# Kernel tuning notes

Measured on AMD Instinct MI355X. Metric: run time of the kernel, lower is better.

## Reference

```python
import jax, jax.numpy as jnp
import numpy as np

# PyTorch LSTM cell with zero initial (h, c): W_hh @ h0 == 0, and c = sigmoid(i)*tanh(g)
# since the forget-gate term f*c0 vanishes. Gate order in torch: i, f, g, o.
# b here is the combined b_ih + b_hh (identical math).

def lstm_step0(x, Wih, b):
    pre = x @ Wih.T + b                      # (N, 4H)
    i, f, g, o = jnp.split(pre, 4, axis=-1)
    c = jax.nn.sigmoid(i) * jnp.tanh(g)
    return jax.nn.sigmoid(o) * jnp.tanh(c)   # (N, H)


def setup_inputs() -> dict:
    key = jax.random.key(0)
    ks = jax.random.split(key, 13)
    num_ts, num_periods, F = 128, 256, 128
    GH, NH, NF = 512, 256, 10
    s = lambda k, shape, fan: (jax.random.normal(k, shape, jnp.float32) / np.sqrt(fan))
    return {
        "X": jax.random.normal(ks[0], (num_ts, num_periods, F), jnp.float32),
        "g_Wih0": s(ks[1], (4 * GH, F), F),
        "g_b0": s(ks[2], (4 * GH,), GH),
        "g_Wih1": s(ks[3], (4 * GH, GH), GH),
        "g_b1": s(ks[4], (4 * GH,), GH),
        "aff_W": s(ks[5], (NF, GH), GH),
        "aff_b": s(ks[6], (NF,), GH),
        "n_Wih0": s(ks[7], (4 * NH, F), F),
        "n_b0": s(ks[8], (4 * NH,), NH),
        "n_Wih1": s(ks[9], (4 * NH, NH), NH),
        "n_b1": s(ks[10], (4 * NH,), NH),
        "noise_W": s(ks[11], (1, NH), NH),
        "noise_b": s(ks[12], (1,), NH),
    }


def reference(X, g_Wih0, g_b0, g_Wih1, g_b1, aff_W, aff_b,
              n_Wih0, n_b0, n_Wih1, n_b1, noise_W, noise_b):
    num_ts, num_periods, num_feats = X.shape
    x = X.reshape(-1, num_feats)             # (num_ts*num_periods, F)

    # Global factor branch: 2-layer LSTM single step from zero state
    hg = lstm_step0(lstm_step0(x, g_Wih0, g_b0), g_Wih1, g_b1)
    hg = jax.nn.relu(hg)
    mus = (hg @ aff_W.T + aff_b).sum(axis=-1).reshape(num_ts, num_periods)

    # Noise branch: 2-layer LSTM single step from zero state
    hn = lstm_step0(lstm_step0(x, n_Wih0, n_b0), n_Wih1, n_b1)
    hn = jax.nn.relu(hn)
    sigmas = jax.nn.softplus(hn @ noise_W.T + noise_b)  # log(1+exp(.)), stable
    sigmas = sigmas.reshape(num_ts, num_periods) + 1e-6
    return mus, sigmas
```

## Files before the change

### kernel.cpp

```cpp
#include <hip/hip_runtime.h>
#include <hip/hip_bf16.h>
#include <hip/hip_fp16.h>

typedef _Float16 h8_t __attribute__((ext_vector_type(8)));
typedef _Float16 h4_t __attribute__((ext_vector_type(4)));
typedef float f4_t __attribute__((ext_vector_type(4)));

#define M_ROWS 32768

__device__ __forceinline__ void gload_lds16(const void* g, void* l) {
  __builtin_amdgcn_global_load_lds((const __attribute__((address_space(1))) void*)g,
                                   (__attribute__((address_space(3))) void*)l, 16, 0, 0);
}

__device__ __forceinline__ float sigmoid_f(float x) { return 1.f / (1.f + __expf(-x)); }
__device__ __forceinline__ float tanh_f(float x) { return 1.f - 2.f / (__expf(2.f * x) + 1.f); }

struct GArgs {
  const _Float16* A;
  const _Float16* W;
  const float* bias;
  _Float16* Hout;
  const float* rvec;
  float* partial;
};

__global__ void prep_all(const float* __restrict__ X, const float* __restrict__ gW0,
                         const float* __restrict__ gW1, const float* __restrict__ nW0,
                         const float* __restrict__ nW1, const float* __restrict__ aff_W,
                         const float* __restrict__ aff_b,
                         _Float16* __restrict__ Xh, _Float16* __restrict__ Wg0,
                         _Float16* __restrict__ Wg1, _Float16* __restrict__ Wn0,
                         _Float16* __restrict__ Wn1,
                         float* __restrict__ pg, float* __restrict__ pn,
                         float* __restrict__ wsum) {
  int b = blockIdx.x;
  const float* s; _Float16* d; int base;
  if (b < 4096)      { s = X;   d = Xh;  base = b; }
  else if (b < 4352) { s = gW0; d = Wg0; base = b - 4096; }
  else if (b < 5376) { s = gW1; d = Wg1; base = b - 4352; }
  else if (b < 5504) { s = nW0; d = Wn0; base = b - 5376; }
  else if (b < 5760) { s = nW1; d = Wn1; base = b - 5504; }
  else if (b < 5888) {
    int i = (b - 5760) * 256 + threadIdx.x;
    pg[i] = 0.f; pn[i] = 0.f;
    return;
  } else {
    int j = (b - 5888) * 256 + threadIdx.x;
    float sum = 0.f;
#pragma unroll
    for (int r = 0; r < 10; ++r) sum += aff_W[r * 512 + j];
    wsum[j] = sum;
    if (j == 0) {
      float bs = 0.f;
#pragma unroll
      for (int r = 0; r < 10; ++r) bs += aff_b[r];
      wsum[512] = bs;
    }
    return;
  }
  int i4 = (base * 256 + threadIdx.x) * 4;
  float4 v = *(const float4*)(s + i4);
  h4_t o;
  o[0] = (_Float16)v.x; o[1] = (_Float16)v.y; o[2] = (_Float16)v.z; o[3] = (_Float16)v.w;
  *(h4_t*)(d + i4) = o;
}

template <int K_DIM, int H_DIM, bool FUSE>
__device__ __forceinline__ void gemm_body(const GArgs& ga, int h0,
                                          _Float16* As, _Float16* Bs) {
  const int tid = threadIdx.x;
  const int wid = tid >> 6;
  const int lane = tid & 63;
  const int wave_m = wid >> 1;
  const int wave_h = wid & 1;
  const int q = lane >> 4;
  const int tcol = lane & 15;
  const int m0 = blockIdx.x * 128;

  const _Float16* aptr[4]; int aoff[4];
#pragma unroll
  for (int c = 0; c < 4; ++c) {
    int o = ((wid * 4 + c) << 10) + (lane << 4);
    int row = o >> 7, pch = (o >> 4) & 7;
    int lch = pch ^ (row & 7);
    aptr[c] = ga.A + (size_t)(m0 + row) * K_DIM + lch * 8;
    aoff[c] = o;
  }
  const _Float16* bptr[6]; int boff[6];
#pragma unroll
  for (int c = 0; c < 6; ++c) {
    int o = ((wid * 6 + c) << 10) + (lane << 4);
    int pan = o >> 13;
    int row = (o >> 7) & 63, pch = (o >> 4) & 7;
    int lch = pch ^ (row & 7);
    int gbase = (pan == 0 ? 0 : (pan == 1 ? 2 * H_DIM : 3 * H_DIM)) + h0 + row;
    bptr[c] = ga.W + (size_t)gbase * K_DIM + lch * 8;
    boff[c] = o;
  }
  int a_rd[2][4];
#pragma unroll
  for (int ks = 0; ks < 2; ++ks)
#pragma unroll
    for (int mi = 0; mi < 4; ++mi) {
      int r = wave_m * 64 + mi * 16 + tcol;
      int c = ks * 4 + q;
      a_rd[ks][mi] = r * 64 + (c ^ (r & 7)) * 8;
    }
  int b_rd[2][2];
#pragma unroll
  for (int ks = 0; ks < 2; ++ks)
#pragma unroll
    for (int ni = 0; ni < 2; ++ni) {
      int j = wave_h * 32 + ni * 16 + tcol;
      int c = ks * 4 + q;
      b_rd[ks][ni] = j * 64 + (c ^ (j & 7)) * 8;
    }

  f4_t acc[3][4][2];
#pragma unroll
  for (int p = 0; p < 3; ++p)
#pragma unroll
    for (int mi = 0; mi < 4; ++mi)
#pragma unroll
      for (int ni = 0; ni < 2; ++ni) acc[p][mi][ni] = (f4_t){0.f, 0.f, 0.f, 0.f};

#pragma unroll
  for (int kk = 0; kk < K_DIM / 64; ++kk) {
#pragma unroll
    for (int c = 0; c < 4; ++c) gload_lds16(aptr[c], (char*)As + aoff[c]);
#pragma unroll
    for (int c = 0; c < 6; ++c) gload_lds16(bptr[c], (char*)Bs + boff[c]);
#pragma unroll
    for (int c = 0; c < 4; ++c) aptr[c] += 64;
#pragma unroll
    for (int c = 0; c < 6; ++c) bptr[c] += 64;
    __syncthreads();

#pragma unroll
    for (int ks = 0; ks < 2; ++ks) {
      h8_t af[4];
#pragma unroll
      for (int mi = 0; mi < 4; ++mi) af[mi] = *(const h8_t*)&As[a_rd[ks][mi]];
#pragma unroll
      for (int p = 0; p < 3; ++p) {
#pragma unroll
        for (int ni = 0; ni < 2; ++ni) {
          h8_t bf = *(const h8_t*)&Bs[p * 4096 + b_rd[ks][ni]];
#pragma unroll
          for (int mi = 0; mi < 4; ++mi)
            acc[p][mi][ni] = __builtin_amdgcn_mfma_f32_16x16x32_f16(af[mi], bf, acc[p][mi][ni], 0, 0, 0);
        }
      }
    }
    __syncthreads();
  }

  const int mrow0 = m0 + wave_m * 64;
  const int jcol0 = h0 + wave_h * 32;

  if constexpr (!FUSE) {
#pragma unroll
    for (int ni = 0; ni < 2; ++ni) {
      int j = jcol0 + ni * 16 + tcol;
      float bi = ga.bias[j];
      float bg = ga.bias[2 * H_DIM + j];
      float bo = ga.bias[3 * H_DIM + j];
#pragma unroll
      for (int mi = 0; mi < 4; ++mi)
#pragma unroll
        for (int r = 0; r < 4; ++r) {
          float pi = acc[0][mi][ni][r] + bi;
          float pgt = acc[1][mi][ni][r] + bg;
          float po = acc[2][mi][ni][r] + bo;
          float cc = sigmoid_f(pi) * tanh_f(pgt);
          float hh = sigmoid_f(po) * tanh_f(cc);
          int m = mrow0 + mi * 16 + q * 4 + r;
          ga.Hout[(size_t)m * H_DIM + j] = (_Float16)hh;
        }
    }
  } else {
    float rsum[4][4];
#pragma unroll
    for (int mi = 0; mi < 4; ++mi)
#pragma unroll
      for (int r = 0; r < 4; ++r) rsum[mi][r] = 0.f;
#pragma unroll
    for (int ni = 0; ni < 2; ++ni) {
      int j = jcol0 + ni * 16 + tcol;
      float bi = ga.bias[j];
      float bg = ga.bias[2 * H_DIM + j];
      float bo = ga.bias[3 * H_DIM + j];
      float rv = ga.rvec[j];
#pragma unroll
      for (int mi = 0; mi < 4; ++mi)
#pragma unroll
        for (int r = 0; r < 4; ++r) {
          float pi = acc[0][mi][ni][r] + bi;
          float pgt = acc[1][mi][ni][r] + bg;
          float po = acc[2][mi][ni][r] + bo;
          float cc = sigmoid_f(pi) * tanh_f(pgt);
          float hh = sigmoid_f(po) * tanh_f(cc);
          hh = fmaxf(hh, 0.f);
          rsum[mi][r] += hh * rv;
        }
    }
#pragma unroll
    for (int mi = 0; mi < 4; ++mi)
#pragma unroll
      for (int r = 0; r < 4; ++r) {
        float v = rsum[mi][r];
        v += __shfl_xor(v, 1);
        v += __shfl_xor(v, 2);
        v += __shfl_xor(v, 4);
        v += __shfl_xor(v, 8);
        if (tcol == 0) atomicAdd(&ga.partial[mrow0 + mi * 16 + q * 4 + r], v);
      }
  }
}

__global__ __launch_bounds__(256, 2) void layer1_fused(GArgs g, GArgs n) {
  __shared__ __align__(16) _Float16 As[128 * 64];
  __shared__ __align__(16) _Float16 Bs[3 * 64 * 64];
  int y = blockIdx.y;
  if (y < 8) gemm_body<128, 512, false>(g, y * 64, As, Bs);
  else       gemm_body<128, 256, false>(n, (y - 8) * 64, As, Bs);
}

__global__ __launch_bounds__(256, 2) void layer2_fused(GArgs g, GArgs n) {
  __shared__ __align__(16) _Float16 As[128 * 64];
  __shared__ __align__(16) _Float16 Bs[3 * 64 * 64];
  int y = blockIdx.y;
  if (y < 8) gemm_body<512, 512, true>(g, y * 64, As, Bs);
  else       gemm_body<256, 256, true>(n, (y - 8) * 64, As, Bs);
}

__global__ void finalize(const float* __restrict__ pg, const float* __restrict__ pn,
                         const float* __restrict__ wsum, const float* __restrict__ noise_b,
                         float* __restrict__ out) {
  int i = blockIdx.x * blockDim.x + threadIdx.x;
  out[i] = pg[i] + wsum[512];
  float x = pn[i] + noise_b[0];
  float sp = fmaxf(x, 0.f) + log1pf(expf(-fabsf(x)));
  out[M_ROWS + i] = sp + 1e-6f;
}

extern "C" void kernel_launch(void* const* d_in, const int* in_sizes, int n_in,
                              void* d_out, int out_size, void* d_ws, size_t ws_size,
                              hipStream_t stream) {
  const float* X       = (const float*)d_in[0];
  const float* g_Wih0  = (const float*)d_in[1];
  const float* g_b0    = (const float*)d_in[2];
  const float* g_Wih1  = (const float*)d_in[3];
  const float* g_b1    = (const float*)d_in[4];
  const float* aff_W   = (const float*)d_in[5];
  const float* aff_b   = (const float*)d_in[6];
  const float* n_Wih0  = (const float*)d_in[7];
  const float* n_b0    = (const float*)d_in[8];
  const float* n_Wih1  = (const float*)d_in[9];
  const float* n_b1    = (const float*)d_in[10];
  const float* noise_W = (const float*)d_in[11];
  const float* noise_b = (const float*)d_in[12];
  float* out = (float*)d_out;

  char* w = (char*)d_ws;
  _Float16* Xh  = (_Float16*)w; w += (size_t)M_ROWS * 128 * 2;
  _Float16* Wg0 = (_Float16*)w; w += 2048 * 128 * 2;
  _Float16* Wg1 = (_Float16*)w; w += 2048 * 512 * 2;
  _Float16* Wn0 = (_Float16*)w; w += 1024 * 128 * 2;
  _Float16* Wn1 = (_Float16*)w; w += 1024 * 256 * 2;
  _Float16* h1g = (_Float16*)w; w += (size_t)M_ROWS * 512 * 2;
  _Float16* h1n = (_Float16*)w; w += (size_t)M_ROWS * 256 * 2;
  float* pg   = (float*)w; w += (size_t)M_ROWS * 4;
  float* pn   = (float*)w; w += (size_t)M_ROWS * 4;
  float* wsum = (float*)w; w += 4096;

  prep_all<<<5890, 256, 0, stream>>>(X, g_Wih0, g_Wih1, n_Wih0, n_Wih1, aff_W, aff_b,
                                     Xh, Wg0, Wg1, Wn0, Wn1, pg, pn, wsum);

  GArgs l1g = {Xh, Wg0, g_b0, h1g, nullptr, nullptr};
  GArgs l1n = {Xh, Wn0, n_b0, h1n, nullptr, nullptr};
  layer1_fused<<<dim3(M_ROWS / 128, 12), 256, 0, stream>>>(l1g, l1n);

  GArgs l2g = {h1g, Wg1, g_b1, nullptr, wsum, pg};
  GArgs l2n = {h1n, Wn1, n_b1, nullptr, noise_W, pn};
  layer2_fused<<<dim3(M_ROWS / 128, 12), 256, 0, stream>>>(l2g, l2n);

  finalize<<<M_ROWS / 256, 256, 0, stream>>>(pg, pn, wsum, noise_b, out);
}
```

Baseline: 299.6 us.

## Double-buffer LDS tiles to overlap global loads with MFMA compute

Doubles the shared-memory A and B tile buffers and restructures the K loop. The next K tile is prefetched with global_load_lds into the alternate buffer while MFMAs run on the current one, and one barrier per iteration is dropped. The aim is to hide global-load latency behind matrix math in both GEMM kernels. LDS per block grows to about 80KB, which may limit occupancy. Layer 1 has only two K iterations, so most of the benefit would come in layer 2.

After: 311.2 us. 1.04x slower.

```diff
diff --git a/kernel.cpp b/kernel.cpp
--- a/kernel.cpp
+++ b/kernel.cpp
@@ -78,6 +78,12 @@
   const int tcol = lane & 15;
   const int m0 = blockIdx.x * 128;
 
+  constexpr int NT = K_DIM / 64;
+  constexpr int A_BYTES = 128 * 64 * 2;
+  constexpr int B_BYTES = 3 * 64 * 64 * 2;
+  constexpr int A_ELEMS = 128 * 64;
+  constexpr int B_ELEMS = 3 * 64 * 64;
+
   const _Float16* aptr[4]; int aoff[4];
 #pragma unroll
   for (int c = 0; c < 4; ++c) {
@@ -126,34 +132,47 @@
       for (int ni = 0; ni < 2; ++ni) acc[p][mi][ni] = (f4_t){0.f, 0.f, 0.f, 0.f};
 
 #pragma unroll
-  for (int kk = 0; kk < K_DIM / 64; ++kk) {
-#pragma unroll
-    for (int c = 0; c < 4; ++c) gload_lds16(aptr[c], (char*)As + aoff[c]);
-#pragma unroll
-    for (int c = 0; c < 6; ++c) gload_lds16(bptr[c], (char*)Bs + boff[c]);
-#pragma unroll
-    for (int c = 0; c < 4; ++c) aptr[c] += 64;
-#pragma unroll
-    for (int c = 0; c < 6; ++c) bptr[c] += 64;
-    __syncthreads();
+  for (int c = 0; c < 4; ++c) gload_lds16(aptr[c], (char*)As + aoff[c]);
+#pragma unroll
+  for (int c = 0; c < 6; ++c) gload_lds16(bptr[c], (char*)Bs + boff[c]);
+#pragma unroll
+  for (int c = 0; c < 4; ++c) aptr[c] += 64;
+#pragma unroll
+  for (int c = 0; c < 6; ++c) bptr[c] += 64;
+  __syncthreads();
+
+#pragma unroll
+  for (int kk = 0; kk < NT; ++kk) {
+    const int cur = kk & 1;
+    const int nxt = cur ^ 1;
+    if (kk < NT - 1) {
+#pragma unroll
+      for (int c = 0; c < 4; ++c) gload_lds16(aptr[c], (char*)As + nxt * A_BYTES + aoff[c]);
+#pragma unroll
+      for (int c = 0; c < 6; ++c) gload_lds16(bptr[c], (char*)Bs + nxt * B_BYTES + boff[c]);
+#pragma unroll
+      for (int c = 0; c < 4; ++c) aptr[c] += 64;
+#pragma unroll
+      for (int c = 0; c < 6; ++c) bptr[c] += 64;
+    }
 
 #pragma unroll
     for (int ks = 0; ks < 2; ++ks) {
       h8_t af[4];
 #pragma unroll
-      for (int mi = 0; mi < 4; ++mi) af[mi] = *(const h8_t*)&As[a_rd[ks][mi]];
+      for (int mi = 0; mi < 4; ++mi) af[mi] = *(const h8_t*)&As[cur * A_ELEMS + a_rd[ks][mi]];
 #pragma unroll
       for (int p = 0; p < 3; ++p) {
 #pragma unroll
         for (int ni = 0; ni < 2; ++ni) {
-          h8_t bf = *(const h8_t*)&Bs[p * 4096 + b_rd[ks][ni]];
+          h8_t bf = *(const h8_t*)&Bs[cur * B_ELEMS + p * 4096 + b_rd[ks][ni]];
 #pragma unroll
           for (int mi = 0; mi < 4; ++mi)
             acc[p][mi][ni] = __builtin_amdgcn_mfma_f32_16x16x32_f16(af[mi], bf, acc[p][mi][ni], 0, 0, 0);
         }
       }
     }
-    __syncthreads();
+    if (kk < NT - 1) __syncthreads();
   }
 
   const int mrow0 = m0 + wave_m * 64;
@@ -220,16 +239,16 @@
 }
 
 __global__ __launch_bounds__(256, 2) void layer1_fused(GArgs g, GArgs n) {
-  __shared__ __align__(16) _Float16 As[128 * 64];
-  __shared__ __align__(16) _Float16 Bs[3 * 64 * 64];
+  __shared__ __align__(16) _Float16 As[2 * 128 * 64];
+  __shared__ __align__(16) _Float16 Bs[2 * 3 * 64 * 64];
   int y = blockIdx.y;
   if (y < 8) gemm_body<128, 512, false>(g, y * 64, As, Bs);
   else       gemm_body<128, 256, false>(n, (y - 8) * 64, As, Bs);
 }
 
 __global__ __launch_bounds__(256, 2) void layer2_fused(GArgs g, GArgs n) {
-  __shared__ __align__(16) _Float16 As[128 * 64];
-  __shared__ __align__(16) _Float16 Bs[3 * 64 * 64];
+  __shared__ __align__(16) _Float16 As[2 * 128 * 64];
+  __shared__ __align__(16) _Float16 Bs[2 * 3 * 64 * 64];
   int y = blockIdx.y;
   if (y < 8) gemm_body<512, 512, true>(g, y * 64, As, Bs);
   else       gemm_body<256, 256, true>(n, (y - 8) * 64, As, Bs);
```
